# Performance work log

Measured on AMD Instinct MI355X. Metric: run time of the kernel, lower is better.

## Reference

```python
import jax, jax.numpy as jnp
import numpy as np

N_NODES = 50000
N_EDGES = 600000
D = 128
L = 3


def setup_inputs() -> dict:
    key = jax.random.key(0)
    ks = jax.random.split(key, 6)
    x = jax.random.normal(ks[0], (N_NODES, D), dtype=jnp.float32)
    edge_index = jax.random.randint(ks[1], (2, N_EDGES), 0, N_NODES, dtype=jnp.int64)
    # Glorot-ish scale for 128x128 linears
    s = 1.0 / np.sqrt(D)
    W_l = jax.random.normal(ks[2], (L, D, D), dtype=jnp.float32) * s
    b_l = jnp.zeros((L, D), dtype=jnp.float32)
    W_r = jax.random.normal(ks[3], (L, D, D), dtype=jnp.float32) * s
    W_out = jax.random.normal(ks[4], (D, 1), dtype=jnp.float32) * s
    b_out = jnp.zeros((1,), dtype=jnp.float32)
    return {"x": x, "edge_index": edge_index, "W_l": W_l, "b_l": b_l,
            "W_r": W_r, "W_out": W_out, "b_out": b_out}


def reference(x, edge_index, W_l, b_l, W_r, W_out, b_out):
    # PyG SAGEConv (aggr='mean', root_weight=True):
    #   out_i = lin_l(mean_{j: (j->i)} x_j) + lin_r(x_i)
    src = edge_index[0]
    dst = edge_index[1]
    n = x.shape[0]
    deg = jax.ops.segment_sum(jnp.ones(src.shape, x.dtype), dst, num_segments=n)
    inv_deg = (1.0 / jnp.maximum(deg, 1.0))[:, None]  # [N,1]
    h = x
    for i in range(W_l.shape[0]):  # fixed small layer count
        agg = jax.ops.segment_sum(h[src], dst, num_segments=n) * inv_deg  # [N,D]
        h = agg @ W_l[i] + b_l[i] + h @ W_r[i]
        h = jax.nn.relu(h)  # dropout is identity at eval (p=0.0)
    return (h @ W_out + b_out)[:, 0]  # squeeze(-1) -> [N]
```

## Files before the change

kernel.cpp:

```cpp
#include <hip/hip_runtime.h>

#define N_NODES 50000
#define N_EDGES 600000
#define D 128
#define NLAYERS 3
#define CSR_CAP (N_EDGES + 3 * N_NODES)

typedef __attribute__((ext_vector_type(8))) short short8;
typedef __attribute__((ext_vector_type(4))) float floatx4;

__device__ __forceinline__ float bf_lo(unsigned u) { return __uint_as_float(u << 16); }
__device__ __forceinline__ float bf_hi(unsigned u) { return __uint_as_float(u & 0xffff0000u); }
__device__ __forceinline__ unsigned short f2bf(float f) {
    unsigned u = __float_as_uint(f);
    return (unsigned short)((u + 0x7fffu + ((u >> 16) & 1u)) >> 16);
}

__device__ __forceinline__ void acc8(float* a, uint4 v) {
    a[0] += bf_lo(v.x); a[1] += bf_hi(v.x);
    a[2] += bf_lo(v.y); a[3] += bf_hi(v.y);
    a[4] += bf_lo(v.z); a[5] += bf_hi(v.z);
    a[6] += bf_lo(v.w); a[7] += bf_hi(v.w);
}


#define CVT_A (N_NODES * D / 4)
#define CVT_B (NLAYERS * D * 256)
#define CVT_TOTAL (CVT_A + CVT_B + N_NODES)

__global__ void cvt_init_kernel(const float* __restrict__ x, const float* __restrict__ Wl,
                                const float* __restrict__ Wr,
                                unsigned short* __restrict__ xb,
                                unsigned short* __restrict__ hb1,
                                unsigned short* __restrict__ hb2,
                                unsigned short* __restrict__ WtF,
                                int* __restrict__ deg, int* __restrict__ cursor,
                                int* __restrict__ counter) {
    int i = blockIdx.x * blockDim.x + threadIdx.x;
    if (i < CVT_A) {
        float4 v = ((const float4*)x)[i];
        ushort4 o;
        o.x = f2bf(v.x); o.y = f2bf(v.y); o.z = f2bf(v.z); o.w = f2bf(v.w);
        ((ushort4*)xb)[i] = o;
    } else if (i < CVT_A + CVT_B) {
        int t = i - CVT_A;
        int l = t >> 15;
        int r = t & 32767;
        int f = r >> 3;
        int ii = r & 7;
        int jkt = f >> 6;
        int lane = f & 63;
        int j = jkt >> 3;
        int kt = jkt & 7;
        int half = lane & 15;
        int quad = lane >> 4;
        int n = j * 16 + half;
        int k = kt * 32 + quad * 8 + ii;
        float v = (k < D) ? Wl[(size_t)l * D * D + (size_t)k * D + n]
                          : Wr[(size_t)l * D * D + (size_t)(k - D) * D + n];
        WtF[t] = f2bf(v);
    } else if (i < CVT_TOTAL) {
        int j = i - (CVT_A + CVT_B);
        deg[j] = 0;
        cursor[j] = 0;
        if (j == 0) counter[0] = 0;
        if (j < D) {
            xb[(size_t)N_NODES * D + j] = 0;
            hb1[(size_t)N_NODES * D + j] = 0;
            hb2[(size_t)N_NODES * D + j] = 0;
        }
    }
}


__global__ void hist_kernel(const int* __restrict__ dst, int* __restrict__ deg) {
    int e = blockIdx.x * blockDim.x + threadIdx.x;
    if (e < N_EDGES) atomicAdd(&deg[dst[e]], 1);
}

__global__ void alloc_kernel(const int* __restrict__ deg, int* __restrict__ counter,
                             int* __restrict__ row_start, float* __restrict__ inv_deg,
                             int* __restrict__ csr_src) {
    int i = blockIdx.x * blockDim.x + threadIdx.x;
    int lane = threadIdx.x & 63;
    int d = (i < N_NODES) ? deg[i] : 0;
    int pd = (d + 3) & ~3;
    int v = pd;
    #pragma unroll
    for (int off = 1; off < 64; off <<= 1) {
        int t = __shfl_up(v, off, 64);
        if (lane >= off) v += t;
    }
    int total = __shfl(v, 63, 64);
    int base = 0;
    if (lane == 63) base = atomicAdd(counter, total);
    base = __shfl(base, 63, 64);
    if (i < N_NODES) {
        int rs = base + v - pd;
        row_start[i] = rs;
        inv_deg[i] = 1.0f / fmaxf((float)d, 1.0f);
        for (int k = d; k < pd; k++) csr_src[rs + k] = N_NODES;
    }
}

__global__ void fill_kernel(const int* __restrict__ src, const int* __restrict__ dst,
                            const int* __restrict__ row_start, int* __restrict__ cursor,
                            int* __restrict__ csr_src) {
    int e = blockIdx.x * blockDim.x + threadIdx.x;
    if (e < N_EDGES) {
        int d_ = dst[e];
        int pos = atomicAdd(&cursor[d_], 1);
        csr_src[row_start[d_] + pos] = src[e];
    }
}


template <bool LAST>
__global__ __launch_bounds__(256) void fused_layer_kernel(
    const unsigned short* __restrict__ hin,
    const int* __restrict__ row_start, const int* __restrict__ deg,
    const int* __restrict__ csr_src, const float* __restrict__ inv_deg,
    const unsigned short* __restrict__ WtF, const float* __restrict__ bias,
    unsigned short* __restrict__ hout,
    const float* __restrict__ Wout, const float* __restrict__ bout,
    float* __restrict__ out) {
    __shared__ unsigned short a_s[32 * 256];
    __shared__ unsigned short c_s[32][136];

    int m0 = blockIdx.x * 32;
    int tid = threadIdx.x;
    int wv = tid >> 6;
    int lane = tid & 63;
    int lane15 = lane & 15;
    int quad = lane >> 4;

    uint4 st0, st1;
    int strow0, stcol0, strow1, stcol1;
    {
        int t0 = tid;
        strow0 = t0 >> 4; stcol0 = t0 & 15;
        int row0 = min(m0 + strow0, N_NODES - 1);
        st0 = *((const uint4*)(hin + (size_t)row0 * D + stcol0 * 8));
        int t1 = 256 + tid;
        strow1 = t1 >> 4; stcol1 = t1 & 15;
        int row1 = min(m0 + strow1, N_NODES - 1);
        st1 = *((const uint4*)(hin + (size_t)row1 * D + stcol1 * 8));
    }

    {
        int nodeBase = m0 + wv * 8;
        int sel = lane & 7;
        int metaIdx = min(nodeBase + sel, N_NODES - 1);
        int rs_l = row_start[metaIdx];
        int dg_l = (nodeBase + sel < N_NODES) ? deg[metaIdx] : 0;
        float w_l = inv_deg[metaIdx];

        int beg_n = __shfl(rs_l, 0, 8);
        int pd_n  = (__shfl(dg_l, 0, 8) + 3) & ~3;
        int idx_next = csr_src[min(beg_n + min(lane15, max(min(pd_n, 16) - 1, 0)),
                                   CSR_CAP - 1)];

        #pragma unroll 1
        for (int n = 0; n < 8; n++) {
            int beg = beg_n;
            int pd  = pd_n;
            int idx = idx_next;
            int n2 = min(n + 1, 7);
            beg_n = __shfl(rs_l, n2, 8);
            pd_n  = (__shfl(dg_l, n2, 8) + 3) & ~3;
            idx_next = csr_src[min(beg_n + min(lane15, max(min(pd_n, 16) - 1, 0)),
                                   CSR_CAP - 1)];

            float a[8] = {0.f, 0.f, 0.f, 0.f, 0.f, 0.f, 0.f, 0.f};

            {
                int cnt = min(pd, 16);
                int nb = cnt >> 2;
                int s0 = __shfl(idx, quad, 16);
                int s1 = __shfl(idx, 4 + quad, 16);
                int s2 = __shfl(idx, 8 + quad, 16);
                int s3 = __shfl(idx, 12 + quad, 16);
                uint4 v0, v1, v2, v3;
                if (nb > 0) v0 = *((const uint4*)(hin + (size_t)s0 * D + lane15 * 8));
                if (nb > 1) v1 = *((const uint4*)(hin + (size_t)s1 * D + lane15 * 8));
                if (nb > 2) v2 = *((const uint4*)(hin + (size_t)s2 * D + lane15 * 8));
                if (nb > 3) v3 = *((const uint4*)(hin + (size_t)s3 * D + lane15 * 8));
                if (nb > 0) acc8(a, v0);
                if (nb > 1) acc8(a, v1);
                if (nb > 2) acc8(a, v2);
                if (nb > 3) acc8(a, v3);
            }
            for (int e = beg + 16; e < beg + pd; e += 16) {
                int cnt = min(beg + pd - e, 16);
                int idx2 = csr_src[e + min(lane15, cnt - 1)];
                int nb = cnt >> 2;
                int s0 = __shfl(idx2, quad, 16);
                int s1 = __shfl(idx2, 4 + quad, 16);
                int s2 = __shfl(idx2, 8 + quad, 16);
                int s3 = __shfl(idx2, 12 + quad, 16);
                uint4 v0, v1, v2, v3;
                if (nb > 0) v0 = *((const uint4*)(hin + (size_t)s0 * D + lane15 * 8));
                if (nb > 1) v1 = *((const uint4*)(hin + (size_t)s1 * D + lane15 * 8));
                if (nb > 2) v2 = *((const uint4*)(hin + (size_t)s2 * D + lane15 * 8));
                if (nb > 3) v3 = *((const uint4*)(hin + (size_t)s3 * D + lane15 * 8));
                if (nb > 0) acc8(a, v0);
                if (nb > 1) acc8(a, v1);
                if (nb > 2) acc8(a, v2);
                if (nb > 3) acc8(a, v3);
            }

            #pragma unroll
            for (int i = 0; i < 8; i++) {
                a[i] += __shfl_xor(a[i], 16, 64);
                a[i] += __shfl_xor(a[i], 32, 64);
            }

            float w = __shfl(w_l, n, 8);
            if (quad == 0) {
                int nl = wv * 8 + n;
                uint4 o;
                o.x = (unsigned)f2bf(a[0] * w) | ((unsigned)f2bf(a[1] * w) << 16);
                o.y = (unsigned)f2bf(a[2] * w) | ((unsigned)f2bf(a[3] * w) << 16);
                o.z = (unsigned)f2bf(a[4] * w) | ((unsigned)f2bf(a[5] * w) << 16);
                o.w = (unsigned)f2bf(a[6] * w) | ((unsigned)f2bf(a[7] * w) << 16);
                int chunk = lane15 ^ (nl & 7);
                *((uint4*)&a_s[nl * 256 + chunk * 8]) = o;
            }
        }
    }

    {
        int chunk0 = (16 + stcol0) ^ (strow0 & 7);
        *((uint4*)&a_s[strow0 * 256 + chunk0 * 8]) = st0;
        int chunk1 = (16 + stcol1) ^ (strow1 & 7);
        *((uint4*)&a_s[strow1 * 256 + chunk1 * 8]) = st1;
    }
    __syncthreads();

    int half = lane15;

    floatx4 acc[2][2];
    #pragma unroll
    for (int mt = 0; mt < 2; mt++)
        #pragma unroll
        for (int jj = 0; jj < 2; jj++)
            acc[mt][jj] = (floatx4){0.f, 0.f, 0.f, 0.f};

    const short8* Bf = (const short8*)WtF;
    #pragma unroll
    for (int kt = 0; kt < 8; kt++) {
        int ch = (kt * 4 + quad) ^ (half & 7);
        short8 a0 = *((const short8*)&a_s[half * 256 + ch * 8]);
        short8 a1 = *((const short8*)&a_s[(16 + half) * 256 + ch * 8]);
        #pragma unroll
        for (int jj = 0; jj < 2; jj++) {
            int j = wv * 2 + jj;
            short8 b = Bf[(j * 8 + kt) * 64 + lane];
            acc[0][jj] = __builtin_amdgcn_mfma_f32_16x16x32_bf16(a0, b, acc[0][jj], 0, 0, 0);
            acc[1][jj] = __builtin_amdgcn_mfma_f32_16x16x32_bf16(a1, b, acc[1][jj], 0, 0, 0);
        }
    }

    if (!LAST) {
        #pragma unroll
        for (int jj = 0; jj < 2; jj++) {
            int col = (wv * 2 + jj) * 16 + half;
            float bv = bias[col];
            #pragma unroll
            for (int mt = 0; mt < 2; mt++)
                #pragma unroll
                for (int r = 0; r < 4; r++)
                    c_s[mt * 16 + quad * 4 + r][col] = f2bf(fmaxf(acc[mt][jj][r] + bv, 0.f));
        }
        __syncthreads();
        #pragma unroll
        for (int it = 0; it < 2; ++it) {
            int t = it * 256 + tid;
            int rl = t >> 4;
            int c = t & 15;
            int row = m0 + rl;
            if (row < N_NODES)
                *((uint4*)(hout + (size_t)row * D + c * 8)) = *((const uint4*)&c_s[rl][c * 8]);
        }
    } else {
        float* red = (float*)&c_s[0][0];
        float vout[2][4] = {{0.f, 0.f, 0.f, 0.f}, {0.f, 0.f, 0.f, 0.f}};
        #pragma unroll
        for (int jj = 0; jj < 2; jj++) {
            int col = (wv * 2 + jj) * 16 + half;
            float bv = bias[col];
            float wo = Wout[col];
            #pragma unroll
            for (int mt = 0; mt < 2; mt++)
                #pragma unroll
                for (int r = 0; r < 4; r++)
                    vout[mt][r] += fmaxf(acc[mt][jj][r] + bv, 0.f) * wo;
        }
        #pragma unroll
        for (int off = 1; off < 16; off <<= 1) {
            #pragma unroll
            for (int mt = 0; mt < 2; mt++)
                #pragma unroll
                for (int r = 0; r < 4; r++)
                    vout[mt][r] += __shfl_xor(vout[mt][r], off, 64);
        }
        if (half == 0) {
            #pragma unroll
            for (int mt = 0; mt < 2; mt++)
                #pragma unroll
                for (int r = 0; r < 4; r++)
                    red[(mt * 16 + quad * 4 + r) * 4 + wv] = vout[mt][r];
        }
        __syncthreads();
        if (tid < 32) {
            int row = m0 + tid;
            if (row < N_NODES)
                out[row] = red[tid * 4 + 0] + red[tid * 4 + 1] +
                           red[tid * 4 + 2] + red[tid * 4 + 3] + bout[0];
        }
    }
}


extern "C" void kernel_launch(void* const* d_in, const int* in_sizes, int n_in,
                              void* d_out, int out_size, void* d_ws, size_t ws_size,
                              hipStream_t stream) {
    const float* x     = (const float*)d_in[0];
    const int*   edge  = (const int*)d_in[1];
    const float* W_l   = (const float*)d_in[2];
    const float* b_l   = (const float*)d_in[3];
    const float* W_r   = (const float*)d_in[4];
    const float* W_out = (const float*)d_in[5];
    const float* b_out = (const float*)d_in[6];
    float* out = (float*)d_out;

    char* ws = (char*)d_ws;
    size_t off = 0;
    auto alloc = [&](size_t bytes) -> void* {
        void* p = ws + off;
        off += (bytes + 255) & ~(size_t)255;
        return p;
    };
    unsigned short* xb  = (unsigned short*)alloc((size_t)(N_NODES + 1) * D * 2);
    unsigned short* hb1 = (unsigned short*)alloc((size_t)(N_NODES + 1) * D * 2);
    unsigned short* hb2 = (unsigned short*)alloc((size_t)(N_NODES + 1) * D * 2);
    unsigned short* WtF = (unsigned short*)alloc((size_t)NLAYERS * D * 256 * 2);
    int*   deg       = (int*)alloc((size_t)N_NODES * sizeof(int));
    int*   row_start = (int*)alloc((size_t)N_NODES * sizeof(int));
    int*   cursor    = (int*)alloc((size_t)N_NODES * sizeof(int));
    float* inv_deg   = (float*)alloc((size_t)N_NODES * sizeof(float));
    int*   csr_src   = (int*)alloc((size_t)CSR_CAP * sizeof(int));
    int*   counter   = (int*)alloc(256);

    const int* src = edge;
    const int* dst = edge + N_EDGES;

    cvt_init_kernel<<<(CVT_TOTAL + 255) / 256, 256, 0, stream>>>(
        x, W_l, W_r, xb, hb1, hb2, WtF, deg, cursor, counter);
    hist_kernel<<<(N_EDGES + 255) / 256, 256, 0, stream>>>(dst, deg);
    alloc_kernel<<<(N_NODES + 255) / 256, 256, 0, stream>>>(deg, counter, row_start, inv_deg, csr_src);
    fill_kernel<<<(N_EDGES + 255) / 256, 256, 0, stream>>>(src, dst, row_start, cursor, csr_src);

    const int grid = (N_NODES + 31) / 32;

    fused_layer_kernel<false><<<grid, 256, 0, stream>>>(
        xb, row_start, deg, csr_src, inv_deg, WtF, b_l, hb1, W_out, b_out, out);
    fused_layer_kernel<false><<<grid, 256, 0, stream>>>(
        hb1, row_start, deg, csr_src, inv_deg, WtF + (size_t)1 * D * 256, b_l + 1 * D,
        hb2, W_out, b_out, out);
    fused_layer_kernel<true><<<grid, 256, 0, stream>>>(
        hb2, row_start, deg, csr_src, inv_deg, WtF + (size_t)2 * D * 256, b_l + 2 * D,
        hb1, W_out, b_out, out);
}
```

Baseline: 243.9 us.

## Stream flattened edge list per wave with double-buffered gathers, drop CSR padding

Replaces the per-node neighbor gather with a flat stream over the contiguous edge range of a wave's 8 nodes. Each lane loads 4 bytes of each source row, and batches of 16 loads are double-buffered so the next batch is in flight while the current one is accumulated. A node's sum is written to shared memory when the stream crosses its end. CSR rows are no longer padded to multiples of 4 and the zero dummy node rows are removed; a small zeroed tail after the edge list keeps over-reads safe. This targets idle time from low memory-level parallelism and from padded or partial batches, at the cost of narrower per-lane loads and a per-edge uniform branch for node boundaries.

```diff
diff --git a/kernel.cpp b/kernel.cpp
--- a/kernel.cpp
+++ b/kernel.cpp
@@ -4,7 +4,7 @@
 #define N_EDGES 600000
 #define D 128
 #define NLAYERS 3
-#define CSR_CAP (N_EDGES + 3 * N_NODES)
+#define CSR_CAP (N_EDGES + 64)
 
 typedef __attribute__((ext_vector_type(8))) short short8;
 typedef __attribute__((ext_vector_type(4))) float floatx4;
@@ -16,13 +16,6 @@
     return (unsigned short)((u + 0x7fffu + ((u >> 16) & 1u)) >> 16);
 }
 
-__device__ __forceinline__ void acc8(float* a, uint4 v) {
-    a[0] += bf_lo(v.x); a[1] += bf_hi(v.x);
-    a[2] += bf_lo(v.y); a[3] += bf_hi(v.y);
-    a[4] += bf_lo(v.z); a[5] += bf_hi(v.z);
-    a[6] += bf_lo(v.w); a[7] += bf_hi(v.w);
-}
-
 
 #define CVT_A (N_NODES * D / 4)
 #define CVT_B (NLAYERS * D * 256)
@@ -31,11 +24,9 @@
 __global__ void cvt_init_kernel(const float* __restrict__ x, const float* __restrict__ Wl,
                                 const float* __restrict__ Wr,
                                 unsigned short* __restrict__ xb,
-                                unsigned short* __restrict__ hb1,
-                                unsigned short* __restrict__ hb2,
                                 unsigned short* __restrict__ WtF,
                                 int* __restrict__ deg, int* __restrict__ cursor,
-                                int* __restrict__ counter) {
+                                int* __restrict__ counter, int* __restrict__ csr_src) {
     int i = blockIdx.x * blockDim.x + threadIdx.x;
     if (i < CVT_A) {
         float4 v = ((const float4*)x)[i];
@@ -64,11 +55,7 @@
         deg[j] = 0;
         cursor[j] = 0;
         if (j == 0) counter[0] = 0;
-        if (j < D) {
-            xb[(size_t)N_NODES * D + j] = 0;
-            hb1[(size_t)N_NODES * D + j] = 0;
-            hb2[(size_t)N_NODES * D + j] = 0;
-        }
+        if (j < 64) csr_src[N_EDGES + j] = 0;
     }
 }
 
@@ -79,13 +66,11 @@
 }
 
 __global__ void alloc_kernel(const int* __restrict__ deg, int* __restrict__ counter,
-                             int* __restrict__ row_start, float* __restrict__ inv_deg,
-                             int* __restrict__ csr_src) {
+                             int* __restrict__ row_start, float* __restrict__ inv_deg) {
     int i = blockIdx.x * blockDim.x + threadIdx.x;
     int lane = threadIdx.x & 63;
     int d = (i < N_NODES) ? deg[i] : 0;
-    int pd = (d + 3) & ~3;
-    int v = pd;
+    int v = d;
     #pragma unroll
     for (int off = 1; off < 64; off <<= 1) {
         int t = __shfl_up(v, off, 64);
@@ -96,10 +81,8 @@
     if (lane == 63) base = atomicAdd(counter, total);
     base = __shfl(base, 63, 64);
     if (i < N_NODES) {
-        int rs = base + v - pd;
-        row_start[i] = rs;
+        row_start[i] = base + v - d;
         inv_deg[i] = 1.0f / fmaxf((float)d, 1.0f);
-        for (int k = d; k < pd; k++) csr_src[rs + k] = N_NODES;
     }
 }
 
@@ -150,83 +133,73 @@
     {
         int nodeBase = m0 + wv * 8;
         int sel = lane & 7;
-        int metaIdx = min(nodeBase + sel, N_NODES - 1);
-        int rs_l = row_start[metaIdx];
-        int dg_l = (nodeBase + sel < N_NODES) ? deg[metaIdx] : 0;
-        float w_l = inv_deg[metaIdx];
-
-        int beg_n = __shfl(rs_l, 0, 8);
-        int pd_n  = (__shfl(dg_l, 0, 8) + 3) & ~3;
-        int idx_next = csr_src[min(beg_n + min(lane15, max(min(pd_n, 16) - 1, 0)),
-                                   CSR_CAP - 1)];
-
-        #pragma unroll 1
-        for (int n = 0; n < 8; n++) {
-            int beg = beg_n;
-            int pd  = pd_n;
-            int idx = idx_next;
-            int n2 = min(n + 1, 7);
-            beg_n = __shfl(rs_l, n2, 8);
-            pd_n  = (__shfl(dg_l, n2, 8) + 3) & ~3;
-            idx_next = csr_src[min(beg_n + min(lane15, max(min(pd_n, 16) - 1, 0)),
-                                   CSR_CAP - 1)];
-
-            float a[8] = {0.f, 0.f, 0.f, 0.f, 0.f, 0.f, 0.f, 0.f};
-
-            {
-                int cnt = min(pd, 16);
-                int nb = cnt >> 2;
-                int s0 = __shfl(idx, quad, 16);
-                int s1 = __shfl(idx, 4 + quad, 16);
-                int s2 = __shfl(idx, 8 + quad, 16);
-                int s3 = __shfl(idx, 12 + quad, 16);
-                uint4 v0, v1, v2, v3;
-                if (nb > 0) v0 = *((const uint4*)(hin + (size_t)s0 * D + lane15 * 8));
-                if (nb > 1) v1 = *((const uint4*)(hin + (size_t)s1 * D + lane15 * 8));
-                if (nb > 2) v2 = *((const uint4*)(hin + (size_t)s2 * D + lane15 * 8));
-                if (nb > 3) v3 = *((const uint4*)(hin + (size_t)s3 * D + lane15 * 8));
-                if (nb > 0) acc8(a, v0);
-                if (nb > 1) acc8(a, v1);
-                if (nb > 2) acc8(a, v2);
-                if (nb > 3) acc8(a, v3);
+        int node = nodeBase + sel;
+        int mi = min(node, N_NODES - 1);
+        int rs = row_start[mi];
+        int dg = (node < N_NODES) ? deg[mi] : 0;
+        float wl = inv_deg[mi];
+        int en = rs + dg;
+
+        int beg = __builtin_amdgcn_readfirstlane(rs);
+        int e = en;
+        e = max(e, __shfl_xor(e, 1, 8));
+        e = max(e, __shfl_xor(e, 2, 8));
+        e = max(e, __shfl_xor(e, 4, 8));
+        int end7 = __builtin_amdgcn_readfirstlane(e);
+        int nb = (end7 - beg + 15) >> 4;
+        if (nb < 1) nb = 1;
+
+        int laneByte = lane << 2;
+        const char* hinB = (const char*)hin;
+
+        float accLo = 0.f, accHi = 0.f;
+        int cur = 0;
+        int endc = __builtin_amdgcn_readfirstlane(__shfl(en, 0, 8));
+        float wc = __shfl(wl, 0, 8);
+        int p = beg;
+
+        unsigned bufA[16], bufB[16];
+
+        auto issue = [&](unsigned* buf, int pb) {
+            #pragma unroll
+            for (int jj = 0; jj < 16; jj++) {
+                int idx = csr_src[pb + jj];
+                buf[jj] = *(const unsigned*)(hinB + ((size_t)(unsigned)idx << 8) + laneByte);
             }
-            for (int e = beg + 16; e < beg + pd; e += 16) {
-                int cnt = min(beg + pd - e, 16);
-                int idx2 = csr_src[e + min(lane15, cnt - 1)];
-                int nb = cnt >> 2;
-                int s0 = __shfl(idx2, quad, 16);
-                int s1 = __shfl(idx2, 4 + quad, 16);
-                int s2 = __shfl(idx2, 8 + quad, 16);
-                int s3 = __shfl(idx2, 12 + quad, 16);
-                uint4 v0, v1, v2, v3;
-                if (nb > 0) v0 = *((const uint4*)(hin + (size_t)s0 * D + lane15 * 8));
-                if (nb > 1) v1 = *((const uint4*)(hin + (size_t)s1 * D + lane15 * 8));
-                if (nb > 2) v2 = *((const uint4*)(hin + (size_t)s2 * D + lane15 * 8));
-                if (nb > 3) v3 = *((const uint4*)(hin + (size_t)s3 * D + lane15 * 8));
-                if (nb > 0) acc8(a, v0);
-                if (nb > 1) acc8(a, v1);
-                if (nb > 2) acc8(a, v2);
-                if (nb > 3) acc8(a, v3);
+        };
+        auto flushNode = [&]() {
+            unsigned o = (unsigned)f2bf(accLo * wc) | ((unsigned)f2bf(accHi * wc) << 16);
+            int nl = wv * 8 + cur;
+            int addr = nl * 512 + ((((lane >> 2) ^ (nl & 7))) << 4) + ((lane & 3) << 2);
+            *(unsigned*)((char*)a_s + addr) = o;
+            cur++;
+            accLo = 0.f; accHi = 0.f;
+            endc = __builtin_amdgcn_readfirstlane(__shfl(en, cur & 7, 8));
+            wc = __shfl(wl, cur & 7, 8);
+        };
+        auto consume = [&](unsigned* buf) {
+            #pragma unroll
+            for (int jj = 0; jj < 16; jj++) {
+                if (p < end7) {
+                    while (cur < 8 && p >= endc) flushNode();
+                    unsigned u = buf[jj];
+                    accLo += bf_lo(u);
+                    accHi += bf_hi(u);
+                }
+                p++;
             }
-
-            #pragma unroll
-            for (int i = 0; i < 8; i++) {
-                a[i] += __shfl_xor(a[i], 16, 64);
-                a[i] += __shfl_xor(a[i], 32, 64);
-            }
-
-            float w = __shfl(w_l, n, 8);
-            if (quad == 0) {
-                int nl = wv * 8 + n;
-                uint4 o;
-                o.x = (unsigned)f2bf(a[0] * w) | ((unsigned)f2bf(a[1] * w) << 16);
-                o.y = (unsigned)f2bf(a[2] * w) | ((unsigned)f2bf(a[3] * w) << 16);
-                o.z = (unsigned)f2bf(a[4] * w) | ((unsigned)f2bf(a[5] * w) << 16);
-                o.w = (unsigned)f2bf(a[6] * w) | ((unsigned)f2bf(a[7] * w) << 16);
-                int chunk = lane15 ^ (nl & 7);
-                *((uint4*)&a_s[nl * 256 + chunk * 8]) = o;
-            }
-        }
+        };
+
+        issue(bufA, beg);
+        int pl = beg + 16;
+        bool curA = true;
+        for (int b = 1; b < nb; b++) {
+            if (curA) { issue(bufB, pl); consume(bufA); }
+            else      { issue(bufA, pl); consume(bufB); }
+            pl += 16; curA = !curA;
+        }
+        if (curA) consume(bufA); else consume(bufB);
+        while (cur < 8) flushNode();
     }
 
     {
@@ -341,9 +314,9 @@
         off += (bytes + 255) & ~(size_t)255;
         return p;
     };
-    unsigned short* xb  = (unsigned short*)alloc((size_t)(N_NODES + 1) * D * 2);
-    unsigned short* hb1 = (unsigned short*)alloc((size_t)(N_NODES + 1) * D * 2);
-    unsigned short* hb2 = (unsigned short*)alloc((size_t)(N_NODES + 1) * D * 2);
+    unsigned short* xb  = (unsigned short*)alloc((size_t)N_NODES * D * 2);
+    unsigned short* hb1 = (unsigned short*)alloc((size_t)N_NODES * D * 2);
+    unsigned short* hb2 = (unsigned short*)alloc((size_t)N_NODES * D * 2);
     unsigned short* WtF = (unsigned short*)alloc((size_t)NLAYERS * D * 256 * 2);
     int*   deg       = (int*)alloc((size_t)N_NODES * sizeof(int));
     int*   row_start = (int*)alloc((size_t)N_NODES * sizeof(int));
@@ -356,9 +329,9 @@
     const int* dst = edge + N_EDGES;
 
     cvt_init_kernel<<<(CVT_TOTAL + 255) / 256, 256, 0, stream>>>(
-        x, W_l, W_r, xb, hb1, hb2, WtF, deg, cursor, counter);
+        x, W_l, W_r, xb, WtF, deg, cursor, counter, csr_src);
     hist_kernel<<<(N_EDGES + 255) / 256, 256, 0, stream>>>(dst, deg);
-    alloc_kernel<<<(N_NODES + 255) / 256, 256, 0, stream>>>(deg, counter, row_start, inv_deg, csr_src);
+    alloc_kernel<<<(N_NODES + 255) / 256, 256, 0, stream>>>(deg, counter, row_start, inv_deg);
     fill_kernel<<<(N_EDGES + 255) / 256, 256, 0, stream>>>(src, dst, row_start, cursor, csr_src);
 
     const int grid = (N_NODES + 31) / 32;
```

New measurement: 250.8 us. +2.8%, slower.
